# Performance work log

Measured on AMD Instinct MI355X. Metric: run time of the kernel, lower is better.

Reference implementation:

```python
import jax, jax.numpy as jnp
import numpy as np

BATCH_SIZE = 8192   # args.batch_size
NUM_VIEWS = 2       # args.num_views
TEMPERATURE = 0.07  # args.loss_args['temperature']
FEAT_DIM = 256
N = (BATCH_SIZE // 2) * NUM_VIEWS  # rows of features


def _static_index_maps():
    # labels = sorted cat of num_views copies of arange(batch_size//2)
    labels = np.sort(np.tile(np.arange(BATCH_SIZE // 2), NUM_VIEWS))
    lab_mat = labels[None, :] == labels[:, None]          # (N, N) bool
    # off-diagonal column indices: for row i, columns [0..N-1] excluding i,
    # in ascending order (matches torch boolean-mask extraction order)
    j = np.arange(N - 1)
    cols = j[None, :] + (j[None, :] >= np.arange(N)[:, None])  # (N, N-1)
    lab_off = np.take_along_axis(lab_mat, cols, axis=1)        # (N, N-1) bool
    k = NUM_VIEWS - 1  # positives per row
    # stable sort puts positive positions first, preserving column order
    order = np.argsort(~lab_off, axis=1, kind='stable')
    pos_cols = order[:, :k]   # (N, k)
    neg_cols = order[:, k:]   # (N, N-1-k)
    return cols, pos_cols, neg_cols

_COLS, _POS_COLS, _NEG_COLS = _static_index_maps()


def setup_inputs() -> dict:
    key = jax.random.key(0)
    features = jax.random.normal(key, (N, FEAT_DIM), dtype=jnp.float32)
    return {"features": features}


def reference(features):
    # L2 normalize rows (F.normalize eps clamp)
    norm = jnp.maximum(jnp.linalg.norm(features, axis=1, keepdims=True), 1e-12)
    f = features / norm
    sim = f @ f.T                                            # (N, N)
    sim_off = jnp.take_along_axis(sim, jnp.asarray(_COLS), axis=1)       # (N, N-1)
    positives = jnp.take_along_axis(sim_off, jnp.asarray(_POS_COLS), axis=1)
    negatives = jnp.take_along_axis(sim_off, jnp.asarray(_NEG_COLS), axis=1)
    logits = jnp.concatenate([positives, negatives], axis=1) / TEMPERATURE
    # CrossEntropyLoss with target class 0 for every row
    loss = jnp.mean(-jax.nn.log_softmax(logits, axis=1)[:, 0])
    return loss
```

## Files before the change

### kernel.cpp

```cpp
#include <hip/hip_runtime.h>
#include <stdint.h>

#define N_ROWS 8192
#define FEAT   256
#define YSPLIT 16
#define CPB    (N_ROWS / YSPLIT)
#define CT     64

typedef __bf16 bf16x8 __attribute__((ext_vector_type(8)));
typedef float  f32x4  __attribute__((ext_vector_type(4)));

__device__ __forceinline__ unsigned short f2bf(float x) {
    union { float f; uint32_t u; } v; v.f = x;
    uint32_t u = v.u;
    return (unsigned short)((u + 0x7FFFu + ((u >> 16) & 1u)) >> 16);
}

__device__ __forceinline__ void gld16(const unsigned short* g, unsigned short* l) {
    __builtin_amdgcn_global_load_lds((__attribute__((address_space(1))) void*)g,
                                     (__attribute__((address_space(3))) void*)l,
                                     16, 0, 0);
}

__global__ void knorm(const float* __restrict__ feat,
                      unsigned short* __restrict__ fb,
                      float* __restrict__ pos) {
    __shared__ float ex[4][FEAT];
    int wave = threadIdx.x >> 6;
    int lane = threadIdx.x & 63;
    int row  = blockIdx.x * 4 + wave;
    float4 v = ((const float4*)(feat + row * FEAT))[lane];
    float ss = v.x*v.x + v.y*v.y + v.z*v.z + v.w*v.w;
    #pragma unroll
    for (int off = 1; off < 64; off <<= 1) ss += __shfl_xor(ss, off);
    float inv = 1.0f / fmaxf(sqrtf(ss), 1e-12f);
    float4 o; o.x = v.x*inv; o.y = v.y*inv; o.z = v.z*inv; o.w = v.w*inv;
    ushort4 b;
    b.x = f2bf(o.x); b.y = f2bf(o.y); b.z = f2bf(o.z); b.w = f2bf(o.w);
    int sidx = (((lane >> 1) ^ (row & 7)) << 1) | (lane & 1);
    ((ushort4*)(fb + row * FEAT))[sidx] = b;
    ((float4*)ex[wave])[lane] = o;
    __syncthreads();
    float4 p = ((float4*)ex[wave ^ 1])[lane];
    float d = o.x*p.x + o.y*p.y + o.z*p.z + o.w*p.w;
    #pragma unroll
    for (int off = 1; off < 64; off <<= 1) d += __shfl_xor(d, off);
    if (lane == 0) pos[row] = d;
}

__global__ __launch_bounds__(256, 1)
void kmain(const unsigned short* __restrict__ fb, float* __restrict__ partial) {
    __shared__ unsigned short bufA[CT * FEAT];
    __shared__ unsigned short bufB[CT * FEAT];
    const int t    = threadIdx.x;
    const int lane = t & 63;
    const int wave = t >> 6;
    const int quad = lane >> 4;
    const int l15  = lane & 15;
    const int rw    = blockIdx.x * 256 + wave * 64;
    const int cbase = blockIdx.y * CPB;
    const float Kc = 20.60992915555662f;

#define STAGE(DST, CC0) do {                                                  \
    const unsigned short* sp_ = fb + (size_t)(cbase + (CC0)) * FEAT + t * 8;  \
    unsigned short* dp_ = (DST) + t * 8;                                      \
    _Pragma("unroll")                                                         \
    for (int i_ = 0; i_ < 8; ++i_)                                            \
        gld16(sp_ + i_ * 2048, dp_ + i_ * 2048);                              \
} while (0)

    STAGE(bufA, 0);

    bf16x8 af[4][8];
    #pragma unroll
    for (int rf = 0; rf < 4; ++rf)
        #pragma unroll
        for (int ks = 0; ks < 8; ++ks) {
            int row = rw + rf * 16 + l15;
            int ch  = (ks * 4 + quad) ^ (row & 7);
            af[rf][ks] = *(const bf16x8*)(fb + row * FEAT + ch * 8);
        }

    float lsum[4][4] = {{0.f,0.f,0.f,0.f},{0.f,0.f,0.f,0.f},
                        {0.f,0.f,0.f,0.f},{0.f,0.f,0.f,0.f}};

#define EPI(AC, RF) do {                                                      \
    const int rb_ = rw + (RF) * 16;                                           \
    const bool dg_ = (cg == rb_);          \
    _Pragma("unroll")                                                         \
    for (int r_ = 0; r_ < 4; ++r_) {                                          \
        float e_ = __builtin_amdgcn_exp2f(fmaf((AC)[r_], Kc, -Kc));           \
        if (dg_ && (rb_ + quad * 4 + r_ == C)) e_ = 0.f;     \
        lsum[(RF)][r_] += e_;                                                 \
    }                                                                         \
} while (0)

#define COMPUTE(BS, CC0) do {                                                 \
    _Pragma("unroll")                                                         \
    for (int g = 0; g < 4; ++g) {                                             \
        const int cg = cbase + (CC0) + g * 16;                                \
        const int C  = cg + l15;                                              \
        f32x4 ac0 = {0.f,0.f,0.f,0.f};                                        \
        f32x4 ac1 = {0.f,0.f,0.f,0.f};                                        \
        f32x4 ac2 = {0.f,0.f,0.f,0.f};                                        \
        f32x4 ac3 = {0.f,0.f,0.f,0.f};                                        \
        _Pragma("unroll")                                                     \
        for (int ks = 0; ks < 8; ++ks) {                                      \
            bf16x8 b = *(const bf16x8*)((BS) + (g * 16 + l15) * FEAT          \
                                        + (((ks * 4 + quad) ^ (l15 & 7)) * 8)); \
            ac0 = __builtin_amdgcn_mfma_f32_16x16x32_bf16(af[0][ks], b, ac0, 0, 0, 0); \
            ac1 = __builtin_amdgcn_mfma_f32_16x16x32_bf16(af[1][ks], b, ac1, 0, 0, 0); \
            ac2 = __builtin_amdgcn_mfma_f32_16x16x32_bf16(af[2][ks], b, ac2, 0, 0, 0); \
            ac3 = __builtin_amdgcn_mfma_f32_16x16x32_bf16(af[3][ks], b, ac3, 0, 0, 0); \
        }                                                                     \
        EPI(ac0, 0); EPI(ac1, 1); EPI(ac2, 2); EPI(ac3, 3);                   \
    }                                                                         \
} while (0)

    asm volatile("s_waitcnt vmcnt(0)" ::: "memory");
    __builtin_amdgcn_s_barrier();
    for (int ct2 = 0; ct2 < CPB / CT; ct2 += 2) {
        STAGE(bufB, (ct2 + 1) * CT);
        COMPUTE(bufA, ct2 * CT);
        asm volatile("s_waitcnt vmcnt(0)" ::: "memory");
        __builtin_amdgcn_s_barrier();
        if (ct2 + 2 < CPB / CT) STAGE(bufA, (ct2 + 2) * CT);
        COMPUTE(bufB, (ct2 + 1) * CT);
        asm volatile("s_waitcnt vmcnt(0)" ::: "memory");
        __builtin_amdgcn_s_barrier();
    }

    #pragma unroll
    for (int rf = 0; rf < 4; ++rf)
        #pragma unroll
        for (int r = 0; r < 4; ++r) {
            float v = lsum[rf][r];
            v += __shfl_xor(v, 1);
            v += __shfl_xor(v, 2);
            v += __shfl_xor(v, 4);
            v += __shfl_xor(v, 8);
            lsum[rf][r] = v;
        }
    if (l15 == 0) {
        #pragma unroll
        for (int rf = 0; rf < 4; ++rf)
            #pragma unroll
            for (int r = 0; r < 4; ++r) {
                int row = rw + rf * 16 + quad * 4 + r;
                partial[blockIdx.y * N_ROWS + row] = lsum[rf][r];
            }
    }
#undef STAGE
#undef COMPUTE
#undef EPI
}

__global__ void kreduce(const float* __restrict__ partial,
                        const float* __restrict__ pos,
                        float* __restrict__ bsum) {
    __shared__ float red[4];
    int row  = blockIdx.x * 256 + threadIdx.x;
    int wave = threadIdx.x >> 6;
    int lane = threadIdx.x & 63;
    float L = 0.f;
    #pragma unroll
    for (int p = 0; p < YSPLIT; ++p) L += partial[p * N_ROWS + row];
    const float invT = 14.285714285714286f;
    float loss = invT * (1.0f - pos[row])
               + 0.6931471805599453f * __builtin_amdgcn_logf(L);
    #pragma unroll
    for (int off = 1; off < 64; off <<= 1) loss += __shfl_xor(loss, off);
    if (lane == 0) red[wave] = loss;
    __syncthreads();
    if (threadIdx.x == 0)
        bsum[blockIdx.x] = red[0] + red[1] + red[2] + red[3];
}

__global__ void kfinal(const float* __restrict__ bsum, float* __restrict__ out) {
    int lane = threadIdx.x;
    float v = (lane < 32) ? bsum[lane] : 0.f;
    #pragma unroll
    for (int off = 1; off < 32; off <<= 1) v += __shfl_xor(v, off);
    if (lane == 0) out[0] = v * (1.0f / 8192.0f);
}

extern "C" void kernel_launch(void* const* d_in, const int* in_sizes, int n_in,
                              void* d_out, int out_size, void* d_ws, size_t ws_size,
                              hipStream_t stream) {
    const float* feat = (const float*)d_in[0];
    float* out = (float*)d_out;
    char* ws = (char*)d_ws;
    unsigned short* fb      = (unsigned short*)ws;
    float*          partial = (float*)(ws + (4u << 20));
    float*          pos     = (float*)(ws + (4u << 20) + (1u << 19));
    float*          bsum    = (float*)(ws + (4u << 20) + (1u << 19) + (1u << 15));

    knorm<<<N_ROWS / 4, 256, 0, stream>>>(feat, fb, pos);
    kmain<<<dim3(32, YSPLIT), 256, 0, stream>>>(fb, partial);
    kreduce<<<N_ROWS / 256, 256, 0, stream>>>(partial, pos, bsum);
    kfinal<<<1, 64, 0, stream>>>(bsum, out);
}
```

Before: 102.2 us.

## Exploit symmetry of similarity matrix by computing only upper-triangular block pairs

The similarity matrix is symmetric, so the kernel now runs only the upper-triangular 256x256 block pairs, each split into two 128-column halves. Each block accumulates both row sums and column sums of exp(logits), so one tile fills in partial sums for both row block a and column block b. This roughly halves the MFMA and exp work. In exchange it adds column reductions through LDS, a while-loop pair decode, more partial slots (64) for the reduce kernel to read, and zero-fill writes for the unused slots.

```diff
diff --git a/kernel.cpp b/kernel.cpp
--- a/kernel.cpp
+++ b/kernel.cpp
@@ -3,8 +3,10 @@
 
 #define N_ROWS 8192
 #define FEAT   256
-#define YSPLIT 16
-#define CPB    (N_ROWS / YSPLIT)
+#define RB     256
+#define NB     (N_ROWS / RB)
+#define NPAIR  (NB * (NB + 1) / 2)
+#define NSLOT  (2 * NB)
 #define CT     64
 
 typedef __bf16 bf16x8 __attribute__((ext_vector_type(8)));
@@ -52,13 +54,22 @@
 void kmain(const unsigned short* __restrict__ fb, float* __restrict__ partial) {
     __shared__ unsigned short bufA[CT * FEAT];
     __shared__ unsigned short bufB[CT * FEAT];
+    __shared__ float colred[4][128];
     const int t    = threadIdx.x;
     const int lane = t & 63;
     const int wave = t >> 6;
     const int quad = lane >> 4;
     const int l15  = lane & 15;
-    const int rw    = blockIdx.x * 256 + wave * 64;
-    const int cbase = blockIdx.y * CPB;
+
+    const int pair = blockIdx.x >> 1;
+    const int h    = blockIdx.x & 1;
+    int a = 0, rem = pair;
+    while (rem >= NB - a) { rem -= NB - a; ++a; }
+    const int b = a + rem;
+    const bool isdiag = (a == b);
+
+    const int rw    = a * RB + wave * 64;
+    const int cbase = b * RB + h * 128;
     const float Kc = 20.60992915555662f;
 
 #define STAGE(DST, CC0) do {                                                  \
@@ -83,19 +94,21 @@
 
     float lsum[4][4] = {{0.f,0.f,0.f,0.f},{0.f,0.f,0.f,0.f},
                         {0.f,0.f,0.f,0.f},{0.f,0.f,0.f,0.f}};
-
-#define EPI(AC, RF) do {                                                      \
+    float cs[8] = {0.f,0.f,0.f,0.f,0.f,0.f,0.f,0.f};
+
+#define EPI(AC, RF, G) do {                                                   \
     const int rb_ = rw + (RF) * 16;                                           \
-    const bool dg_ = (cg == rb_);          \
+    const bool dg_ = (cg == rb_);        \
     _Pragma("unroll")                                                         \
     for (int r_ = 0; r_ < 4; ++r_) {                                          \
         float e_ = __builtin_amdgcn_exp2f(fmaf((AC)[r_], Kc, -Kc));           \
         if (dg_ && (rb_ + quad * 4 + r_ == C)) e_ = 0.f;     \
         lsum[(RF)][r_] += e_;                                                 \
+        cs[(G)] += e_;                                                        \
     }                                                                         \
 } while (0)
 
-#define COMPUTE(BS, CC0) do {                                                 \
+#define COMPUTE(BS, CC0, CS0) do {                                            \
     _Pragma("unroll")                                                         \
     for (int g = 0; g < 4; ++g) {                                             \
         const int cg = cbase + (CC0) + g * 16;                                \
@@ -106,30 +119,27 @@
         f32x4 ac3 = {0.f,0.f,0.f,0.f};                                        \
         _Pragma("unroll")                                                     \
         for (int ks = 0; ks < 8; ++ks) {                                      \
-            bf16x8 b = *(const bf16x8*)((BS) + (g * 16 + l15) * FEAT          \
+            bf16x8 bv = *(const bf16x8*)((BS) + (g * 16 + l15) * FEAT         \
                                         + (((ks * 4 + quad) ^ (l15 & 7)) * 8)); \
-            ac0 = __builtin_amdgcn_mfma_f32_16x16x32_bf16(af[0][ks], b, ac0, 0, 0, 0); \
-            ac1 = __builtin_amdgcn_mfma_f32_16x16x32_bf16(af[1][ks], b, ac1, 0, 0, 0); \
-            ac2 = __builtin_amdgcn_mfma_f32_16x16x32_bf16(af[2][ks], b, ac2, 0, 0, 0); \
-            ac3 = __builtin_amdgcn_mfma_f32_16x16x32_bf16(af[3][ks], b, ac3, 0, 0, 0); \
+            ac0 = __builtin_amdgcn_mfma_f32_16x16x32_bf16(af[0][ks], bv, ac0, 0, 0, 0); \
+            ac1 = __builtin_amdgcn_mfma_f32_16x16x32_bf16(af[1][ks], bv, ac1, 0, 0, 0); \
+            ac2 = __builtin_amdgcn_mfma_f32_16x16x32_bf16(af[2][ks], bv, ac2, 0, 0, 0); \
+            ac3 = __builtin_amdgcn_mfma_f32_16x16x32_bf16(af[3][ks], bv, ac3, 0, 0, 0); \
         }                                                                     \
-        EPI(ac0, 0); EPI(ac1, 1); EPI(ac2, 2); EPI(ac3, 3);                   \
+        EPI(ac0, 0, (CS0) + g); EPI(ac1, 1, (CS0) + g);                       \
+        EPI(ac2, 2, (CS0) + g); EPI(ac3, 3, (CS0) + g);                       \
     }                                                                         \
 } while (0)
 
     asm volatile("s_waitcnt vmcnt(0)" ::: "memory");
     __builtin_amdgcn_s_barrier();
-    for (int ct2 = 0; ct2 < CPB / CT; ct2 += 2) {
-        STAGE(bufB, (ct2 + 1) * CT);
-        COMPUTE(bufA, ct2 * CT);
-        asm volatile("s_waitcnt vmcnt(0)" ::: "memory");
-        __builtin_amdgcn_s_barrier();
-        if (ct2 + 2 < CPB / CT) STAGE(bufA, (ct2 + 2) * CT);
-        COMPUTE(bufB, (ct2 + 1) * CT);
-        asm volatile("s_waitcnt vmcnt(0)" ::: "memory");
-        __builtin_amdgcn_s_barrier();
-    }
-
+    STAGE(bufB, CT);
+    COMPUTE(bufA, 0, 0);
+    asm volatile("s_waitcnt vmcnt(0)" ::: "memory");
+    __builtin_amdgcn_s_barrier();
+    COMPUTE(bufB, CT, 4);
+
+    const int rslot = 2 * b + h;
     #pragma unroll
     for (int rf = 0; rf < 4; ++rf)
         #pragma unroll
@@ -147,8 +157,25 @@
             #pragma unroll
             for (int r = 0; r < 4; ++r) {
                 int row = rw + rf * 16 + quad * 4 + r;
-                partial[blockIdx.y * N_ROWS + row] = lsum[rf][r];
+                partial[rslot * N_ROWS + row] = lsum[rf][r];
             }
+    }
+
+    #pragma unroll
+    for (int g = 0; g < 8; ++g) {
+        float v = cs[g];
+        v += __shfl_xor(v, 16);
+        v += __shfl_xor(v, 32);
+        if (lane < 16) colred[wave][g * 16 + l15] = v;
+    }
+    __syncthreads();
+    if (!isdiag && t < 128) {
+        float s = colred[0][t] + colred[1][t] + colred[2][t] + colred[3][t];
+        partial[(2 * a) * N_ROWS + b * RB + h * 128 + t] = s;
+    }
+    if (isdiag && h == 0) {
+        for (int j = 0; j < a; ++j)
+            partial[(2 * j + 1) * N_ROWS + a * RB + t] = 0.f;
     }
 #undef STAGE
 #undef COMPUTE
@@ -164,7 +191,7 @@
     int lane = threadIdx.x & 63;
     float L = 0.f;
     #pragma unroll
-    for (int p = 0; p < YSPLIT; ++p) L += partial[p * N_ROWS + row];
+    for (int p = 0; p < NSLOT; ++p) L += partial[p * N_ROWS + row];
     const float invT = 14.285714285714286f;
     float loss = invT * (1.0f - pos[row])
                + 0.6931471805599453f * __builtin_amdgcn_logf(L);
@@ -192,11 +219,11 @@
     char* ws = (char*)d_ws;
     unsigned short* fb      = (unsigned short*)ws;
     float*          partial = (float*)(ws + (4u << 20));
-    float*          pos     = (float*)(ws + (4u << 20) + (1u << 19));
-    float*          bsum    = (float*)(ws + (4u << 20) + (1u << 19) + (1u << 15));
+    float*          pos     = (float*)(ws + (6u << 20));
+    float*          bsum    = (float*)(ws + (6u << 20) + (1u << 15));
 
     knorm<<<N_ROWS / 4, 256, 0, stream>>>(feat, fb, pos);
-    kmain<<<dim3(32, YSPLIT), 256, 0, stream>>>(fb, partial);
+    kmain<<<NPAIR * 2, 256, 0, stream>>>(fb, partial);
     kreduce<<<N_ROWS / 256, 256, 0, stream>>>(partial, pos, bsum);
     kfinal<<<1, 64, 0, stream>>>(bsum, out);
 }
```

Result: slower. 121.1 us (+18.5%).

## Software-pipeline exp epilogue of previous column group with next group's MFMAs

Applied to the files above, without the earlier changes.

Restructures the per-tile compute so the exp/accumulate epilogue for column group g-1 is interleaved between the MFMA k-steps of group g, using double-buffered accumulator sets. It also raises wave priority around the MFMA sequences with s_setprio. The aim is to hide the transcendental VALU epilogue latency behind matrix-core work. It costs 16 more live accumulator registers, which may increase register pressure in a kernel already holding a large A fragment array.

```diff
diff --git a/kernel.cpp b/kernel.cpp
--- a/kernel.cpp
+++ b/kernel.cpp
@@ -84,48 +84,91 @@
     float lsum[4][4] = {{0.f,0.f,0.f,0.f},{0.f,0.f,0.f,0.f},
                         {0.f,0.f,0.f,0.f},{0.f,0.f,0.f,0.f}};
 
-#define EPI(AC, RF) do {                                                      \
-    const int rb_ = rw + (RF) * 16;                                           \
-    const bool dg_ = (cg == rb_);          \
-    _Pragma("unroll")                                                         \
-    for (int r_ = 0; r_ < 4; ++r_) {                                          \
-        float e_ = __builtin_amdgcn_exp2f(fmaf((AC)[r_], Kc, -Kc));           \
-        if (dg_ && (rb_ + quad * 4 + r_ == C)) e_ = 0.f;     \
-        lsum[(RF)][r_] += e_;                                                 \
-    }                                                                         \
-} while (0)
-
-#define COMPUTE(BS, CC0) do {                                                 \
-    _Pragma("unroll")                                                         \
-    for (int g = 0; g < 4; ++g) {                                             \
-        const int cg = cbase + (CC0) + g * 16;                                \
-        const int C  = cg + l15;                                              \
-        f32x4 ac0 = {0.f,0.f,0.f,0.f};                                        \
-        f32x4 ac1 = {0.f,0.f,0.f,0.f};                                        \
-        f32x4 ac2 = {0.f,0.f,0.f,0.f};                                        \
-        f32x4 ac3 = {0.f,0.f,0.f,0.f};                                        \
-        _Pragma("unroll")                                                     \
-        for (int ks = 0; ks < 8; ++ks) {                                      \
-            bf16x8 b = *(const bf16x8*)((BS) + (g * 16 + l15) * FEAT          \
-                                        + (((ks * 4 + quad) ^ (l15 & 7)) * 8)); \
-            ac0 = __builtin_amdgcn_mfma_f32_16x16x32_bf16(af[0][ks], b, ac0, 0, 0, 0); \
-            ac1 = __builtin_amdgcn_mfma_f32_16x16x32_bf16(af[1][ks], b, ac1, 0, 0, 0); \
-            ac2 = __builtin_amdgcn_mfma_f32_16x16x32_bf16(af[2][ks], b, ac2, 0, 0, 0); \
-            ac3 = __builtin_amdgcn_mfma_f32_16x16x32_bf16(af[3][ks], b, ac3, 0, 0, 0); \
-        }                                                                     \
-        EPI(ac0, 0); EPI(ac1, 1); EPI(ac2, 2); EPI(ac3, 3);                   \
-    }                                                                         \
+#define KSTEP(BS, G, KS, W0, W1, W2, W3) do {                                 \
+    bf16x8 bv_ = *(const bf16x8*)((BS) + ((G) * 16 + l15) * FEAT              \
+                                  + ((((KS) * 4 + quad) ^ (l15 & 7)) * 8));   \
+    W0 = __builtin_amdgcn_mfma_f32_16x16x32_bf16(af[0][KS], bv_, W0, 0, 0, 0);\
+    W1 = __builtin_amdgcn_mfma_f32_16x16x32_bf16(af[1][KS], bv_, W1, 0, 0, 0);\
+    W2 = __builtin_amdgcn_mfma_f32_16x16x32_bf16(af[2][KS], bv_, W2, 0, 0, 0);\
+    W3 = __builtin_amdgcn_mfma_f32_16x16x32_bf16(af[3][KS], bv_, W3, 0, 0, 0);\
+} while (0)
+
+#define EPI_ONE(C0, GP, RF, RI, AC) do {                                      \
+    const int cgp_ = (C0) + (GP) * 16;                                        \
+    const bool dgp_ = (cgp_ == rw + (RF) * 16);   \
+    float e_ = __builtin_amdgcn_exp2f(fmaf((AC)[RI], Kc, -Kc));               \
+    if (dgp_ && (rw + (RF) * 16 + quad * 4 + (RI) == cgp_ + l15)) e_ = 0.f;   \
+    lsum[RF][RI] += e_;                                                       \
+} while (0)
+
+#define GRP0(BS, C0, G, W0, W1, W2, W3) do {                                  \
+    W0 = (f32x4){0.f,0.f,0.f,0.f}; W1 = (f32x4){0.f,0.f,0.f,0.f};             \
+    W2 = (f32x4){0.f,0.f,0.f,0.f}; W3 = (f32x4){0.f,0.f,0.f,0.f};             \
+    __builtin_amdgcn_s_setprio(1);                                            \
+    KSTEP(BS, G, 0, W0, W1, W2, W3);                                          \
+    KSTEP(BS, G, 1, W0, W1, W2, W3);                                          \
+    KSTEP(BS, G, 2, W0, W1, W2, W3);                                          \
+    KSTEP(BS, G, 3, W0, W1, W2, W3);                                          \
+    KSTEP(BS, G, 4, W0, W1, W2, W3);                                          \
+    KSTEP(BS, G, 5, W0, W1, W2, W3);                                          \
+    KSTEP(BS, G, 6, W0, W1, W2, W3);                                          \
+    KSTEP(BS, G, 7, W0, W1, W2, W3);                                          \
+    __builtin_amdgcn_s_setprio(0);                                            \
+} while (0)
+
+#define GRP(BS, C0, G, W0, W1, W2, W3, GP, R0, R1, R2, R3) do {               \
+    W0 = (f32x4){0.f,0.f,0.f,0.f}; W1 = (f32x4){0.f,0.f,0.f,0.f};             \
+    W2 = (f32x4){0.f,0.f,0.f,0.f}; W3 = (f32x4){0.f,0.f,0.f,0.f};             \
+    __builtin_amdgcn_s_setprio(1);                                            \
+    KSTEP(BS, G, 0, W0, W1, W2, W3);                                          \
+    EPI_ONE(C0, GP, 0, 0, R0); EPI_ONE(C0, GP, 0, 1, R0);                     \
+    KSTEP(BS, G, 1, W0, W1, W2, W3);                                          \
+    EPI_ONE(C0, GP, 0, 2, R0); EPI_ONE(C0, GP, 0, 3, R0);                     \
+    KSTEP(BS, G, 2, W0, W1, W2, W3);                                          \
+    EPI_ONE(C0, GP, 1, 0, R1); EPI_ONE(C0, GP, 1, 1, R1);                     \
+    KSTEP(BS, G, 3, W0, W1, W2, W3);                                          \
+    EPI_ONE(C0, GP, 1, 2, R1); EPI_ONE(C0, GP, 1, 3, R1);                     \
+    KSTEP(BS, G, 4, W0, W1, W2, W3);                                          \
+    EPI_ONE(C0, GP, 2, 0, R2); EPI_ONE(C0, GP, 2, 1, R2);                     \
+    KSTEP(BS, G, 5, W0, W1, W2, W3);                                          \
+    EPI_ONE(C0, GP, 2, 2, R2); EPI_ONE(C0, GP, 2, 3, R2);                     \
+    KSTEP(BS, G, 6, W0, W1, W2, W3);                                          \
+    EPI_ONE(C0, GP, 3, 0, R3); EPI_ONE(C0, GP, 3, 1, R3);                     \
+    KSTEP(BS, G, 7, W0, W1, W2, W3);                                          \
+    EPI_ONE(C0, GP, 3, 2, R3); EPI_ONE(C0, GP, 3, 3, R3);                     \
+    __builtin_amdgcn_s_setprio(0);                                            \
+} while (0)
+
+#define EPI_TAIL(C0, GP, R0, R1, R2, R3) do {                                 \
+    EPI_ONE(C0, GP, 0, 0, R0); EPI_ONE(C0, GP, 0, 1, R0);                     \
+    EPI_ONE(C0, GP, 0, 2, R0); EPI_ONE(C0, GP, 0, 3, R0);                     \
+    EPI_ONE(C0, GP, 1, 0, R1); EPI_ONE(C0, GP, 1, 1, R1);                     \
+    EPI_ONE(C0, GP, 1, 2, R1); EPI_ONE(C0, GP, 1, 3, R1);                     \
+    EPI_ONE(C0, GP, 2, 0, R2); EPI_ONE(C0, GP, 2, 1, R2);                     \
+    EPI_ONE(C0, GP, 2, 2, R2); EPI_ONE(C0, GP, 2, 3, R2);                     \
+    EPI_ONE(C0, GP, 3, 0, R3); EPI_ONE(C0, GP, 3, 1, R3);                     \
+    EPI_ONE(C0, GP, 3, 2, R3); EPI_ONE(C0, GP, 3, 3, R3);                     \
+} while (0)
+
+#define COMPUTE_PIPE(BS, CC0) do {                                            \
+    const int c0_ = cbase + (CC0);                                            \
+    f32x4 A0, A1, A2, A3, B0, B1, B2, B3;                                     \
+    GRP0(BS, c0_, 0, A0, A1, A2, A3);                                         \
+    GRP (BS, c0_, 1, B0, B1, B2, B3, 0, A0, A1, A2, A3);                      \
+    GRP (BS, c0_, 2, A0, A1, A2, A3, 1, B0, B1, B2, B3);                      \
+    GRP (BS, c0_, 3, B0, B1, B2, B3, 2, A0, A1, A2, A3);                      \
+    EPI_TAIL(c0_, 3, B0, B1, B2, B3);                                         \
 } while (0)
 
     asm volatile("s_waitcnt vmcnt(0)" ::: "memory");
     __builtin_amdgcn_s_barrier();
     for (int ct2 = 0; ct2 < CPB / CT; ct2 += 2) {
         STAGE(bufB, (ct2 + 1) * CT);
-        COMPUTE(bufA, ct2 * CT);
+        COMPUTE_PIPE(bufA, ct2 * CT);
         asm volatile("s_waitcnt vmcnt(0)" ::: "memory");
         __builtin_amdgcn_s_barrier();
         if (ct2 + 2 < CPB / CT) STAGE(bufA, (ct2 + 2) * CT);
-        COMPUTE(bufB, (ct2 + 1) * CT);
+        COMPUTE_PIPE(bufB, (ct2 + 1) * CT);
         asm volatile("s_waitcnt vmcnt(0)" ::: "memory");
         __builtin_amdgcn_s_barrier();
     }
@@ -151,8 +194,12 @@
             }
     }
 #undef STAGE
-#undef COMPUTE
-#undef EPI
+#undef KSTEP
+#undef EPI_ONE
+#undef GRP0
+#undef GRP
+#undef EPI_TAIL
+#undef COMPUTE_PIPE
 }
 
 __global__ void kreduce(const float* __restrict__ partial,
```

Result: no change. 100.9 us (-1.2%).
